# Kernel tuning notes

Measured on AMD Instinct MI355X. Metric: run time of the kernel, lower is better.

The kernel has to match this reference:

```python
import jax, jax.numpy as jnp
import numpy as np

B, N_SRC, N_NGH, D, H = 256, 32, 2048, 128, 2
DK = D // H  # 64
FEAT = 128
NEG_INF = -1e10
LN_EPS = 1e-5


def setup_inputs() -> dict:
    key = jax.random.key(0)
    ks = jax.random.split(key, 16)
    inp = {
        "src": jax.random.normal(ks[0], (B, N_SRC, D), jnp.float32),
        "ngh_feat": jax.random.normal(ks[1], (B * N_NGH, D), jnp.float32),
        "hidden": jnp.zeros((B * N_NGH, D), jnp.float32),
        "mask": jax.random.bernoulli(ks[2], 0.5, (B, N_NGH)),
        # GRUCell params (torch layout: [3H, in], gate order r,z,n)
        "gru_w_ih": jax.random.normal(ks[3], (3 * D, D), jnp.float32) * 0.05,
        "gru_w_hh": jax.random.normal(ks[4], (3 * D, D), jnp.float32) * 0.05,
        "gru_b_ih": jnp.zeros((3 * D,), jnp.float32),
        "gru_b_hh": jnp.zeros((3 * D,), jnp.float32),
        # multi-head attention projections (no bias in source)
        "w_qs": jax.random.normal(ks[5], (H * DK, D), jnp.float32) * np.sqrt(2.0 / (D + DK)).astype(np.float32),
        "w_ks": jax.random.normal(ks[6], (H * DK, D), jnp.float32) * np.sqrt(2.0 / (D + DK)).astype(np.float32),
        "w_vs": jax.random.normal(ks[7], (H * DK, D), jnp.float32) * np.sqrt(2.0 / (D + DK)).astype(np.float32),
        "fc_w": jax.random.normal(ks[8], (D, H * DK), jnp.float32) * 0.05,
        "fc_b": jnp.zeros((D,), jnp.float32),
        "ln_g": jnp.ones((D,), jnp.float32),
        "ln_b": jnp.zeros((D,), jnp.float32),
        # MergeLayer(model_dim, model_dim, feat_dim, feat_dim)
        "m_fc1_w": jax.random.normal(ks[9], (FEAT, 2 * D), jnp.float32) * 0.05,
        "m_fc1_b": jnp.zeros((FEAT,), jnp.float32),
        "m_fc2_w": jax.random.normal(ks[10], (FEAT, FEAT), jnp.float32) * 0.05,
        "m_fc2_b": jnp.zeros((FEAT,), jnp.float32),
    }
    return inp


def gru_cell(x, h, w_ih, w_hh, b_ih, b_hh):
    gi = x @ w_ih.T + b_ih
    gh = h @ w_hh.T + b_hh
    ir, iz, in_ = jnp.split(gi, 3, axis=-1)
    hr, hz, hn = jnp.split(gh, 3, axis=-1)
    r = jax.nn.sigmoid(ir + hr)
    z = jax.nn.sigmoid(iz + hz)
    n = jnp.tanh(in_ + r * hn)
    return (1.0 - z) * n + z * h


def reference(src, ngh_feat, hidden, mask,
              gru_w_ih, gru_w_hh, gru_b_ih, gru_b_hh,
              w_qs, w_ks, w_vs, fc_w, fc_b, ln_g, ln_b,
              m_fc1_w, m_fc1_b, m_fc2_w, m_fc2_b):
    b, n_src, d = src.shape
    n_ngh = mask.shape[1]
    nn = n_ngh // n_src  # neighbors per source
    temperature = jnp.sqrt(jnp.float32(DK))

    # GRU walk encoding of neighbor features -> seq [B, N_ngh, D]
    seq = gru_cell(ngh_feat, hidden, gru_w_ih, gru_w_hh, gru_b_ih, gru_b_hh)
    seq = seq.reshape(b, n_ngh, d)

    # grouped multi-head attention (q per source, k/v over its nn neighbors)
    q = (src @ w_qs.T).reshape(b, n_src, H, DK)            # bshd
    k = (seq @ w_ks.T).reshape(b, n_src, nn, H, DK)        # bsnhd
    v = (seq @ w_vs.T).reshape(b, n_src, nn, H, DK)
    scores = jnp.einsum('bshd,bsnhd->bshn', q, k) / temperature
    m = mask.reshape(b, n_src, 1, nn)                      # broadcast over heads
    scores = jnp.where(m, NEG_INF, scores)
    attn = jax.nn.softmax(scores, axis=-1)                 # dropout is eval no-op
    out = jnp.einsum('bshn,bsnhd->bshd', attn, v).reshape(b, n_src, H * DK)
    out = out @ fc_w.T + fc_b

    # residual + layernorm
    x = out + src
    mu = jnp.mean(x, axis=-1, keepdims=True)
    var = jnp.var(x, axis=-1, keepdims=True)
    x = (x - mu) * jax.lax.rsqrt(var + LN_EPS) * ln_g + ln_b

    # MergeLayer: cat + MLP
    cat = jnp.concatenate([x, src], axis=-1)
    h1 = jax.nn.relu(cat @ m_fc1_w.T + m_fc1_b)
    z = h1 @ m_fc2_w.T + m_fc2_b                            # [B, N_src, feat_dim]
    return z
```

## Files before the change

### kernel.cpp

```cpp
#include <hip/hip_runtime.h>

typedef float  f32x4  __attribute__((ext_vector_type(4)));
typedef short  bf16x8 __attribute__((ext_vector_type(8)));
typedef unsigned short u16x4 __attribute__((ext_vector_type(4)));

typedef const __attribute__((address_space(1))) unsigned int* gas_u32;
typedef __attribute__((address_space(3))) unsigned int* las_u32;

#define MFMA16(a,b,c) __builtin_amdgcn_mfma_f32_16x16x32_bf16((a),(b),(c),0,0,0)

__device__ __forceinline__ unsigned short f2bf(float f){
  unsigned u = __float_as_uint(f);
  u += 0x7fffu + ((u>>16)&1u);
  return (unsigned short)(u>>16);
}
__device__ __forceinline__ float bf2f(unsigned short u){
  return __uint_as_float(((unsigned)u)<<16);
}
__device__ __forceinline__ float sigm(float x){
  return __fdividef(1.f, 1.f + __expf(-x));
}
__device__ __forceinline__ float tanhfast(float x){
  return 1.f - __fdividef(2.f, __expf(2.f*x) + 1.f);
}
__device__ __forceinline__ float dot128(const float* __restrict__ w, const float* s){
  float a0=0.f,a1=0.f,a2=0.f,a3=0.f;
  #pragma unroll
  for (int e=0;e<32;++e){
    f32x4 w4 = *(const f32x4*)(w + (e<<2));
    f32x4 x4 = *(const f32x4*)(s + (e<<2));
    a0 = fmaf(w4[0],x4[0],a0); a1 = fmaf(w4[1],x4[1],a1);
    a2 = fmaf(w4[2],x4[2],a2); a3 = fmaf(w4[3],x4[3],a3);
  }
  return (a0+a1)+(a2+a3);
}
__device__ __forceinline__ bf16x8 cvt8(const f32x4 a, const f32x4 b){
  union { int i[4]; bf16x8 v; } u;
  asm("v_cvt_pk_bf16_f32 %0, %1, %2" : "=v"(u.i[0]) : "v"(a[0]), "v"(a[1]));
  asm("v_cvt_pk_bf16_f32 %0, %1, %2" : "=v"(u.i[1]) : "v"(a[2]), "v"(a[3]));
  asm("v_cvt_pk_bf16_f32 %0, %1, %2" : "=v"(u.i[2]) : "v"(b[0]), "v"(b[1]));
  asm("v_cvt_pk_bf16_f32 %0, %1, %2" : "=v"(u.i[3]) : "v"(b[2]), "v"(b[3]));
  return u.v;
}
__device__ __forceinline__ u16x4 pack4(float a, float b, float c, float d){
  union { int i[2]; u16x4 v; } u;
  asm("v_cvt_pk_bf16_f32 %0, %1, %2" : "=v"(u.i[0]) : "v"(a), "v"(b));
  asm("v_cvt_pk_bf16_f32 %0, %1, %2" : "=v"(u.i[1]) : "v"(c), "v"(d));
  return u.v;
}
__device__ __forceinline__ int swx(int m){ return (((m&7)<<1) | ((m>>3)&1)) << 2; }
__device__ __forceinline__ int sws(int m){ return ((m&7)<<3) | (((m>>3)&1)<<6); }

#define XB_OFF   0
#define SEQ_OFF  24576
#define QKB_OFF  40960
#define SC_OFF   43008
#define SH_OFF   43520
#define BIAS_OFF 47616
#define SMEM_SZ  49664

__global__ void prep_all(const float* __restrict__ wih, const float* __restrict__ whh,
                         const float* __restrict__ wqs, const float* __restrict__ wks,
                         const float* __restrict__ wvs, const float* __restrict__ fcw,
                         const float* __restrict__ src, const int* __restrict__ mask_i,
                         const float* __restrict__ hid,
                         unsigned short* __restrict__ wbf, float* __restrict__ M_ws,
                         unsigned short* __restrict__ qk_ws,
                         unsigned long long* __restrict__ mask_bits,
                         int* __restrict__ flags){
  __shared__ __align__(16) float sl_src[32*128];
  __shared__ __align__(16) float sl_q[32*128];
  const int b = blockIdx.x, t = threadIdx.x;
  if (b < 384){
    const int tid = b*256 + t;
    if (tid < 49152) wbf[tid] = f2bf(wih[tid]);
    else             wbf[tid] = f2bf(whh[tid-49152]);
  } else if (b < 512){
    const int tid = (b-384)*256 + t;
    const int h = tid>>14, d = (tid>>7)&127, e = tid&127;
    float a = 0.f;
    for (int j=0;j<64;++j)
      a = fmaf(fcw[d*128 + (h<<6) + j], wvs[((h<<6)+j)*128 + e], a);
    M_ws[tid] = a;
  } else if (b < 768){
    const int blk = b - 512;
    const size_t s0 = (size_t)blk * 32;
    for (int i=0;i<16;++i) sl_src[t + i*256] = src[s0*128 + t + i*256];
    __syncthreads();
    for (int k=0;k<16;++k){
      const int job = t + k*256, s = job>>7, c = job&127;
      sl_q[job] = dot128(wqs + c*128, sl_src + s*128);
    }
    __syncthreads();
    const int d = t&127, h = (t>>7)&1;
    float acc[32];
    #pragma unroll
    for (int s=0;s<32;++s) acc[s]=0.f;
    for (int j=0;j<64;++j){
      const float wk = wks[((h<<6)+j)*128 + d];
      #pragma unroll
      for (int s=0;s<32;++s) acc[s] = fmaf(wk, sl_q[s*128 + (h<<6) + j], acc[s]);
    }
    for (int s=0;s<32;++s) qk_ws[(s0+s)*256 + (h<<7) + d] = f2bf(acc[s]*0.125f);
  } else if (b < 2816){
    const int blk = b - 768;
    const int wv = t>>6, lane = t&63;
    const int gsrc = blk*4 + wv;
    const unsigned v = (unsigned)mask_i[(size_t)gsrc*64 + lane];
    const int bytemode = __any((int)(v > 1u));
    bool bit;
    if (bytemode) bit = (((const unsigned char*)mask_i)[(size_t)gsrc*64 + lane] != 0);
    else          bit = (v != 0u);
    const unsigned long long bits = __ballot((int)bit);
    if (lane == 0) mask_bits[gsrc] = bits;
  } else {
    const size_t blk = b - 2816;
    bool nz = false;
    #pragma unroll 4
    for (int it=0; it<32; ++it){
      const size_t idx = blk*8192 + (size_t)it*256 + t;
      const f32x4 v = *(const f32x4*)(hid + idx*4);
      nz = nz || (v[0]!=0.f)||(v[1]!=0.f)||(v[2]!=0.f)||(v[3]!=0.f);
    }
    if (__ballot((int)nz)){ if ((t&63)==0) atomicOr(flags+1, 1); }
  }
}

__device__ __forceinline__ void scores_pv(char* smem, int srcI, unsigned long long mb,
                                          int wv, int lane, int l15, int lgrp){
  unsigned short* seq = (unsigned short*)(smem + SEQ_OFF);
  const unsigned short* qkb = (const unsigned short*)(smem + QKB_OFF);
  float* sc = (float*)(smem + SC_OFF);
  float* sH = (float*)(smem + SH_OFF);
  const f32x4 z4 = {0.f,0.f,0.f,0.f};
  {
    const int srow = (wv<<4) + l15;
    f32x4 s4 = z4;
    #pragma unroll
    for (int kb=0;kb<4;++kb){
      const int ko = (kb<<5) + (lgrp<<3);
      bf16x8 qa = *(const bf16x8*)&qkb[(srcI<<8) + ((l15&1)<<7) + ko];
      bf16x8 sb = *(const bf16x8*)&seq[(srow<<7) + (ko ^ sws(srow))];
      s4 = MFMA16(qa, sb, s4);
    }
    if (lgrp == 0){
      sc[      (wv<<4) + l15] = s4[0];
      sc[64 +  (wv<<4) + l15] = s4[1];
    }
  }
  asm volatile("s_waitcnt lgkmcnt(0)" ::: "memory");
  __builtin_amdgcn_sched_barrier(0);
  __builtin_amdgcn_s_barrier();
  if (wv < 2){
    float s = ((mb>>lane)&1ull) ? -1e10f : sc[(wv<<6)+lane];
    float mx = s;
    #pragma unroll
    for (int o=32;o>=1;o>>=1) mx = fmaxf(mx, __shfl_xor(mx,o));
    const float e = __expf(s - mx);
    float sum = e;
    #pragma unroll
    for (int o=32;o>=1;o>>=1) sum += __shfl_xor(sum,o);
    sc[(wv<<6)+lane] = __fdividef(e, sum);
  }
  asm volatile("s_waitcnt lgkmcnt(0)" ::: "memory");
  __builtin_amdgcn_sched_barrier(0);
  __builtin_amdgcn_s_barrier();
  {
    const int tt = (wv<<6) + lane;
    const int jidx = tt>>2, sub = tt&3;
    const int hh2 = jidx>>5, quad = jidx&31;
    f32x4 a = z4;
    #pragma unroll
    for (int i=0;i<16;++i){
      const int rr = (sub<<4)+i;
      const u16x4 sv = *(const u16x4*)&seq[(rr<<7) + ((quad<<2) ^ sws(rr))];
      const float w = sc[(hh2<<6)+rr];
      #pragma unroll
      for (int k=0;k<4;++k) a[k] = fmaf(w, bf2f(sv[k]), a[k]);
    }
    #pragma unroll
    for (int k=0;k<4;++k){ a[k] += __shfl_xor(a[k],1); a[k] += __shfl_xor(a[k],2); }
    if (sub == 0)
      *(f32x4*)&sH[(((srcI<<1)+hh2)<<7) + (quad<<2)] = a;
  }
}

__global__ __attribute__((amdgpu_flat_work_group_size(256,256)))
           __attribute__((amdgpu_waves_per_eu(2)))
void cawn_main(
    const float* __restrict__ src, const float* __restrict__ ngh,
    const float* __restrict__ hid,
    const float* __restrict__ bih, const float* __restrict__ bhh,
    const float* __restrict__ fcb, const float* __restrict__ lng,
    const float* __restrict__ lnb, const float* __restrict__ m1w,
    const float* __restrict__ m1b, const float* __restrict__ m2w,
    const float* __restrict__ m2b,
    const unsigned short* __restrict__ wihb, const unsigned short* __restrict__ whhb,
    const float* __restrict__ M_ws, const unsigned short* __restrict__ qk_ws,
    const unsigned long long* __restrict__ mask_bits,
    const int* __restrict__ flags, float* __restrict__ out)
{
  __shared__ __align__(16) char smem[SMEM_SZ];
  float* brz0   = (float*)(smem + BIAS_OFF);
  float* brz1   = (float*)(smem + BIAS_OFF + 512);
  float* bin_l  = (float*)(smem + BIAS_OFF + 1024);
  float* bhn_l  = (float*)(smem + BIAS_OFF + 1536);
  unsigned short* seq = (unsigned short*)(smem + SEQ_OFF);
  unsigned short* qkb = (unsigned short*)(smem + QKB_OFF);

  const int t    = threadIdx.x;
  const int wv   = t >> 6;
  const int lane = t & 63;
  const int l15  = lane & 15;
  const int lgrp = lane >> 4;
  const int gsrc0 = blockIdx.x * 4;
  const f32x4 z4 = {0.f,0.f,0.f,0.f};
  const int hz = flags[1];

  if (t < 128){
    brz0[t]  = bih[t]     + bhh[t];
    brz1[t]  = bih[128+t] + bhh[128+t];
    bin_l[t] = bih[256+t];
    bhn_l[t] = bhh[256+t];
  }
  #pragma unroll
  for (int s=0;s<4;++s)
    qkb[(s<<8)+t] = qk_ws[(size_t)(gsrc0+s)*256 + t];
  const unsigned long long mb0 = mask_bits[gsrc0];
  const unsigned long long mb1 = mask_bits[gsrc0+1];
  const unsigned long long mb2 = mask_bits[gsrc0+2];
  const unsigned long long mb3 = mask_bits[gsrc0+3];

  if (!hz){
    bf16x8 Wf[3][2][4];
    #pragma unroll
    for (int g=0; g<3; ++g)
      #pragma unroll
      for (int j=0; j<2; ++j){
        const int nc = (wv<<5) + (j<<4) + l15;
        #pragma unroll
        for (int kb=0; kb<4; ++kb)
          Wf[g][j][kb] = *(const bf16x8*)(wihb + (((g<<7) + nc)<<7) + (kb<<5) + (lgrp<<3));
      }

    auto issue = [&](int kk, int rbuf){
      const int srcI = kk>>2, stg = kk&3;
      const size_t base = (size_t)(gsrc0+srcI)*8192 + (size_t)stg*2048;
      #pragma unroll
      for (int r=0;r<2;++r){
        const int rl = (wv<<2) + (r<<1) + (lane>>5);
        const int s16 = (lane&31) ^ (((rl&7)<<1) | ((rl>>3)&1));
        const float* g = ngh + base + (rl<<7) + (s16<<2);
        char* l = smem + XB_OFF + rbuf*8192 + (((wv<<2)+(r<<1))<<9);
        __builtin_amdgcn_global_load_lds((gas_u32)g, (las_u32)l, 16, 0, 0);
      }
    };
    issue(0,0); issue(1,1);

    int rb = 0;
    for (int k=0;k<16;++k){
      if (k < 15) asm volatile("s_waitcnt vmcnt(2) lgkmcnt(0)" ::: "memory");
      else        asm volatile("s_waitcnt vmcnt(0) lgkmcnt(0)" ::: "memory");
      __builtin_amdgcn_sched_barrier(0);
      __builtin_amdgcn_s_barrier();
      if (k+2 < 16){
        int ri = rb+2; if (ri>=3) ri-=3;
        issue(k+2, ri);
      }

      const int srcI = k>>2, stg = k&3;
      const float* xrow = (const float*)(smem + XB_OFF + rb*8192) + (l15<<7);
      const int sw = swx(l15);
      bf16x8 bx[4];
      #pragma unroll
      for (int kb=0;kb<4;++kb){
        const int c0 = (kb<<5) + (lgrp<<3);
        bx[kb] = cvt8(*(const f32x4*)&xrow[c0 ^ sw], *(const f32x4*)&xrow[(c0+4) ^ sw]);
      }
      f32x4 ar[2]={z4,z4}, az[2]={z4,z4}, an[2]={z4,z4};
      #pragma unroll
      for (int j=0;j<2;++j)
        #pragma unroll
        for (int kb=0;kb<4;++kb){
          ar[j] = MFMA16(Wf[0][j][kb], bx[kb], ar[j]);
          az[j] = MFMA16(Wf[1][j][kb], bx[kb], az[j]);
          an[j] = MFMA16(Wf[2][j][kb], bx[kb], an[j]);
        }
      const int mrow = (stg<<4) + l15;
      #pragma unroll
      for (int j=0;j<2;++j){
        const int colb = (wv<<5) + (j<<4) + (lgrp<<2);
        const f32x4 b0 = *(const f32x4*)&brz0[colb];
        const f32x4 b1 = *(const f32x4*)&brz1[colb];
        const f32x4 b2 = *(const f32x4*)&bin_l[colb];
        const f32x4 b3 = *(const f32x4*)&bhn_l[colb];
        float o[4];
        #pragma unroll
        for (int i=0;i<4;++i){
          const float rv = sigm(ar[j][i] + b0[i]);
          const float zv = sigm(az[j][i] + b1[i]);
          const float nv = tanhfast(an[j][i] + b2[i] + rv*b3[i]);
          o[i] = (1.f - zv)*nv;
        }
        *(u16x4*)&seq[(mrow<<7) + (colb ^ sws(mrow))] = pack4(o[0],o[1],o[2],o[3]);
      }

      if (stg == 3){
        asm volatile("s_waitcnt lgkmcnt(0)" ::: "memory");
        __builtin_amdgcn_sched_barrier(0);
        __builtin_amdgcn_s_barrier();
        const unsigned long long mb = (srcI==0)?mb0:(srcI==1)?mb1:(srcI==2)?mb2:mb3;
        scores_pv(smem, srcI, mb, wv, lane, l15, lgrp);
      }
      rb = (rb+1 == 3) ? 0 : rb+1;
    }
  } else {
    float* xb0 = (float*)(smem + XB_OFF);
    float* xb1 = (float*)(smem + XB_OFF + 8192);
    for (int srcI=0;srcI<4;++srcI){
      const int gsrc = gsrc0+srcI;
      for (int stg=0;stg<4;++stg){
        #pragma unroll
        for (int it=0; it<2; ++it){
          const int f = t + (it<<8);
          const int m = f>>5, c0 = (f&31)<<2;
          const int sw = swx(m);
          const size_t gb = (size_t)gsrc*8192 + stg*2048 + (m<<7) + c0;
          *(f32x4*)&xb0[(m<<7)+(c0^sw)] = *(const f32x4*)(ngh+gb);
          *(f32x4*)&xb1[(m<<7)+(c0^sw)] = *(const f32x4*)(hid+gb);
        }
        __syncthreads();
        const float* xrow = xb0 + (l15<<7);
        const float* hrow = xb1 + (l15<<7);
        const int sw = swx(l15);
        bf16x8 bx[4], bh[4];
        #pragma unroll
        for (int kb=0;kb<4;++kb){
          const int c0 = (kb<<5) + (lgrp<<3);
          bx[kb] = cvt8(*(const f32x4*)&xrow[c0 ^ sw], *(const f32x4*)&xrow[(c0+4) ^ sw]);
          bh[kb] = cvt8(*(const f32x4*)&hrow[c0 ^ sw], *(const f32x4*)&hrow[(c0+4) ^ sw]);
        }
        f32x4 ar[2]={z4,z4}, az[2]={z4,z4}, an[2]={z4,z4}, anh[2]={z4,z4};
        #pragma unroll
        for (int j=0;j<2;++j){
          const int nc = (wv<<5)+(j<<4)+l15;
          #pragma unroll
          for (int kb=0;kb<4;++kb){
            const int ko=(kb<<5)+(lgrp<<3);
            bf16x8 w0 = *(const bf16x8*)(wihb + ((      nc)<<7) + ko);
            bf16x8 w1 = *(const bf16x8*)(wihb + (((128)+nc)<<7) + ko);
            bf16x8 w2 = *(const bf16x8*)(wihb + (((256)+nc)<<7) + ko);
            ar[j] = MFMA16(w0, bx[kb], ar[j]);
            az[j] = MFMA16(w1, bx[kb], az[j]);
            an[j] = MFMA16(w2, bx[kb], an[j]);
            bf16x8 u0 = *(const bf16x8*)(whhb + ((      nc)<<7) + ko);
            bf16x8 u1 = *(const bf16x8*)(whhb + (((128)+nc)<<7) + ko);
            bf16x8 u2 = *(const bf16x8*)(whhb + (((256)+nc)<<7) + ko);
            ar[j]  = MFMA16(u0, bh[kb], ar[j]);
            az[j]  = MFMA16(u1, bh[kb], az[j]);
            anh[j] = MFMA16(u2, bh[kb], anh[j]);
          }
        }
        const int mrow = (stg<<4) + l15;
        #pragma unroll
        for (int j=0;j<2;++j){
          const int colb = (wv<<5) + (j<<4) + (lgrp<<2);
          const f32x4 b0 = *(const f32x4*)&brz0[colb];
          const f32x4 b1 = *(const f32x4*)&brz1[colb];
          const f32x4 b2 = *(const f32x4*)&bin_l[colb];
          const f32x4 b3 = *(const f32x4*)&bhn_l[colb];
          const f32x4 hv = *(const f32x4*)&hrow[colb ^ sw];
          float o[4];
          #pragma unroll
          for (int i=0;i<4;++i){
            const float rv = sigm(ar[j][i] + b0[i]);
            const float zv = sigm(az[j][i] + b1[i]);
            const float nv = tanhfast(an[j][i] + b2[i] + rv*(anh[j][i] + b3[i]));
            o[i] = (1.f - zv)*nv + zv*hv[i];
          }
          *(u16x4*)&seq[(mrow<<7) + (colb ^ sws(mrow))] = pack4(o[0],o[1],o[2],o[3]);
        }
        __syncthreads();
      }
      const unsigned long long mb = (srcI==0)?mb0:(srcI==1)?mb1:(srcI==2)?mb2:mb3;
      scores_pv(smem, srcI, mb, wv, lane, l15, lgrp);
      __syncthreads();
    }
  }

  __syncthreads();
  float* ep1  = (float*)smem;
  float* ep2  = (float*)(smem + 2048);
  float* srce = (float*)(smem + 4096);
  float* sH   = (float*)(smem + SH_OFF);
  srce[t]     = src[(size_t)gsrc0*128 + t];
  srce[t+256] = src[(size_t)gsrc0*128 + t + 256];
  __syncthreads();

  const int d  = t & 127;
  const int sh = (t >> 7) << 1;
  #pragma unroll
  for (int si=0; si<2; ++si){
    const int s = sh + si;
    float a = fcb[d];
    a += dot128(M_ws +         d*128, &sH[((s<<1)  )<<7]);
    a += dot128(M_ws + 16384 + d*128, &sH[((s<<1)+1)<<7]);
    ep1[s*128+d] = a + srce[s*128+d];
  }
  __syncthreads();
  {
    const int s = wv;
    const float v0 = ep1[s*128+lane], v1 = ep1[s*128+64+lane];
    float sum = v0+v1, sq_ = v0*v0 + v1*v1;
    #pragma unroll
    for (int o=32;o>=1;o>>=1){ sum += __shfl_xor(sum,o); sq_ += __shfl_xor(sq_,o); }
    const float mu  = sum * 0.0078125f;
    const float var = sq_ * 0.0078125f - mu*mu;
    const float rs  = rsqrtf(var + 1e-5f);
    ep1[s*128+lane]    = (v0-mu)*rs*lng[lane]    + lnb[lane];
    ep1[s*128+64+lane] = (v1-mu)*rs*lng[64+lane] + lnb[64+lane];
  }
  __syncthreads();
  #pragma unroll
  for (int si=0; si<2; ++si){
    const int s = sh + si;
    float a = m1b[d];
    a += dot128(m1w + d*256,       ep1  + s*128);
    a += dot128(m1w + d*256 + 128, srce + s*128);
    ep2[s*128+d] = fmaxf(a, 0.f);
  }
  __syncthreads();
  #pragma unroll
  for (int si=0; si<2; ++si){
    const int s = sh + si;
    out[(size_t)(gsrc0+s)*128 + d] = m2b[d] + dot128(m2w + d*128, ep2 + s*128);
  }
}

extern "C" void kernel_launch(void* const* d_in, const int* in_sizes, int n_in,
                              void* d_out, int out_size, void* d_ws, size_t ws_size,
                              hipStream_t stream){
  const float* src = (const float*)d_in[0];
  const float* ngh = (const float*)d_in[1];
  const float* hid = (const float*)d_in[2];
  const int*   msk = (const int*)  d_in[3];
  const float* wih = (const float*)d_in[4];
  const float* whh = (const float*)d_in[5];
  const float* bih = (const float*)d_in[6];
  const float* bhh = (const float*)d_in[7];
  const float* wqs = (const float*)d_in[8];
  const float* wks = (const float*)d_in[9];
  const float* wvs = (const float*)d_in[10];
  const float* fcw = (const float*)d_in[11];
  const float* fcb = (const float*)d_in[12];
  const float* lng = (const float*)d_in[13];
  const float* lnb = (const float*)d_in[14];
  const float* m1w = (const float*)d_in[15];
  const float* m1b = (const float*)d_in[16];
  const float* m2w = (const float*)d_in[17];
  const float* m2b = (const float*)d_in[18];
  float* out = (float*)d_out;

  unsigned short* wbf   = (unsigned short*)d_ws;
  int*            flags = (int*)((char*)d_ws + 196608);
  float*          M_ws  = (float*)((char*)d_ws + 196672);
  unsigned short* qk_ws = (unsigned short*)((char*)d_ws + 327744);
  unsigned long long* mask_bits = (unsigned long long*)((char*)d_ws + 4522048);

  hipMemsetAsync((char*)d_ws + 196608, 0, 64, stream);
  prep_all <<<4864, 256, 0, stream>>>(wih, whh, wqs, wks, wvs, fcw, src, msk, hid,
                                      wbf, M_ws, qk_ws, mask_bits, flags);
  cawn_main<<<2048, 256, 0, stream>>>(src, ngh, hid, bih, bhh,
                                      fcb, lng, lnb, m1w, m1b, m2w, m2b,
                                      wbf, wbf + 49152, M_ws, qk_ws,
                                      mask_bits, flags, out);
}
```

Baseline: 438.6 us.

## Split zero-hidden and general GRU paths into separate kernels, load inputs directly

Splits the main kernel into a fast kernel for the zero-hidden case and a slow kernel for the general case. Each kernel exits early based on a runtime flag. The fast kernel drops the triple-buffered global_load_lds staging of neighbor features and loads them straight from global memory into registers. This cuts shared memory per block from about 49 KB to about 25 KB to raise occupancy, at the cost of losing the async prefetch overlap and adding a second kernel launch that does no work.

Measured after the change: 545.9 us. 24.5% more time.

```diff
diff --git a/kernel.cpp b/kernel.cpp
--- a/kernel.cpp
+++ b/kernel.cpp
@@ -3,9 +3,6 @@
 typedef float  f32x4  __attribute__((ext_vector_type(4)));
 typedef short  bf16x8 __attribute__((ext_vector_type(8)));
 typedef unsigned short u16x4 __attribute__((ext_vector_type(4)));
-
-typedef const __attribute__((address_space(1))) unsigned int* gas_u32;
-typedef __attribute__((address_space(3))) unsigned int* las_u32;
 
 #define MFMA16(a,b,c) __builtin_amdgcn_mfma_f32_16x16x32_bf16((a),(b),(c),0,0,0)
 
@@ -48,16 +45,22 @@
   asm("v_cvt_pk_bf16_f32 %0, %1, %2" : "=v"(u.i[1]) : "v"(c), "v"(d));
   return u.v;
 }
+__device__ __forceinline__ int sws(int m){ return ((m&7)<<3) | (((m>>3)&1)<<6); }
 __device__ __forceinline__ int swx(int m){ return (((m&7)<<1) | ((m>>3)&1)) << 2; }
-__device__ __forceinline__ int sws(int m){ return ((m&7)<<3) | (((m>>3)&1)<<6); }
-
-#define XB_OFF   0
-#define SEQ_OFF  24576
-#define QKB_OFF  40960
-#define SC_OFF   43008
-#define SH_OFF   43520
-#define BIAS_OFF 47616
-#define SMEM_SZ  49664
+
+__device__ __forceinline__ void bar_lgkm(){
+  asm volatile("s_waitcnt lgkmcnt(0)" ::: "memory");
+  __builtin_amdgcn_sched_barrier(0);
+  __builtin_amdgcn_s_barrier();
+}
+
+#define SEQ_OFF  0
+#define QKB_OFF  16384
+#define SC_OFF   18432
+#define SH_OFF   18944
+#define BIAS_OFF 23040
+#define SMEM_FAST 25088
+#define SMEM_SLOW 41472
 
 __global__ void prep_all(const float* __restrict__ wih, const float* __restrict__ whh,
                          const float* __restrict__ wqs, const float* __restrict__ wks,
@@ -148,9 +151,7 @@
       sc[64 +  (wv<<4) + l15] = s4[1];
     }
   }
-  asm volatile("s_waitcnt lgkmcnt(0)" ::: "memory");
-  __builtin_amdgcn_sched_barrier(0);
-  __builtin_amdgcn_s_barrier();
+  bar_lgkm();
   if (wv < 2){
     float s = ((mb>>lane)&1ull) ? -1e10f : sc[(wv<<6)+lane];
     float mx = s;
@@ -162,9 +163,7 @@
     for (int o=32;o>=1;o>>=1) sum += __shfl_xor(sum,o);
     sc[(wv<<6)+lane] = __fdividef(e, sum);
   }
-  asm volatile("s_waitcnt lgkmcnt(0)" ::: "memory");
-  __builtin_amdgcn_sched_barrier(0);
-  __builtin_amdgcn_s_barrier();
+  bar_lgkm();
   {
     const int tt = (wv<<6) + lane;
     const int jidx = tt>>2, sub = tt&3;
@@ -185,22 +184,76 @@
   }
 }
 
+__device__ __forceinline__ void epilogue(char* smem, int t, int wv, int lane, int gsrc0,
+    const float* __restrict__ src, const float* __restrict__ fcb,
+    const float* __restrict__ lng, const float* __restrict__ lnb,
+    const float* __restrict__ m1w, const float* __restrict__ m1b,
+    const float* __restrict__ m2w, const float* __restrict__ m2b,
+    const float* __restrict__ M_ws, float* __restrict__ out){
+  float* ep1  = (float*)smem;
+  float* ep2  = (float*)(smem + 2048);
+  float* srce = (float*)(smem + 4096);
+  float* sH   = (float*)(smem + SH_OFF);
+  srce[t]     = src[(size_t)gsrc0*128 + t];
+  srce[t+256] = src[(size_t)gsrc0*128 + t + 256];
+  __syncthreads();
+
+  const int d  = t & 127;
+  const int sh = (t >> 7) << 1;
+  #pragma unroll
+  for (int si=0; si<2; ++si){
+    const int s = sh + si;
+    float a = fcb[d];
+    a += dot128(M_ws +         d*128, &sH[((s<<1)  )<<7]);
+    a += dot128(M_ws + 16384 + d*128, &sH[((s<<1)+1)<<7]);
+    ep1[s*128+d] = a + srce[s*128+d];
+  }
+  __syncthreads();
+  {
+    const int s = wv;
+    const float v0 = ep1[s*128+lane], v1 = ep1[s*128+64+lane];
+    float sum = v0+v1, sq_ = v0*v0 + v1*v1;
+    #pragma unroll
+    for (int o=32;o>=1;o>>=1){ sum += __shfl_xor(sum,o); sq_ += __shfl_xor(sq_,o); }
+    const float mu  = sum * 0.0078125f;
+    const float var = sq_ * 0.0078125f - mu*mu;
+    const float rs  = rsqrtf(var + 1e-5f);
+    ep1[s*128+lane]    = (v0-mu)*rs*lng[lane]    + lnb[lane];
+    ep1[s*128+64+lane] = (v1-mu)*rs*lng[64+lane] + lnb[64+lane];
+  }
+  __syncthreads();
+  #pragma unroll
+  for (int si=0; si<2; ++si){
+    const int s = sh + si;
+    float a = m1b[d];
+    a += dot128(m1w + d*256,       ep1  + s*128);
+    a += dot128(m1w + d*256 + 128, srce + s*128);
+    ep2[s*128+d] = fmaxf(a, 0.f);
+  }
+  __syncthreads();
+  #pragma unroll
+  for (int si=0; si<2; ++si){
+    const int s = sh + si;
+    out[(size_t)(gsrc0+s)*128 + d] = m2b[d] + dot128(m2w + d*128, ep2 + s*128);
+  }
+}
+
 __global__ __attribute__((amdgpu_flat_work_group_size(256,256)))
            __attribute__((amdgpu_waves_per_eu(2)))
-void cawn_main(
+void cawn_fast(
     const float* __restrict__ src, const float* __restrict__ ngh,
-    const float* __restrict__ hid,
     const float* __restrict__ bih, const float* __restrict__ bhh,
     const float* __restrict__ fcb, const float* __restrict__ lng,
     const float* __restrict__ lnb, const float* __restrict__ m1w,
     const float* __restrict__ m1b, const float* __restrict__ m2w,
     const float* __restrict__ m2b,
-    const unsigned short* __restrict__ wihb, const unsigned short* __restrict__ whhb,
+    const unsigned short* __restrict__ wihb,
     const float* __restrict__ M_ws, const unsigned short* __restrict__ qk_ws,
     const unsigned long long* __restrict__ mask_bits,
     const int* __restrict__ flags, float* __restrict__ out)
 {
-  __shared__ __align__(16) char smem[SMEM_SZ];
+  if (flags[1]) return;
+  __shared__ __align__(16) char smem[SMEM_FAST];
   float* brz0   = (float*)(smem + BIAS_OFF);
   float* brz1   = (float*)(smem + BIAS_OFF + 512);
   float* bin_l  = (float*)(smem + BIAS_OFF + 1024);
@@ -215,7 +268,6 @@
   const int lgrp = lane >> 4;
   const int gsrc0 = blockIdx.x * 4;
   const f32x4 z4 = {0.f,0.f,0.f,0.f};
-  const int hz = flags[1];
 
   if (t < 128){
     brz0[t]  = bih[t]     + bhh[t];
@@ -226,57 +278,29 @@
   #pragma unroll
   for (int s=0;s<4;++s)
     qkb[(s<<8)+t] = qk_ws[(size_t)(gsrc0+s)*256 + t];
-  const unsigned long long mb0 = mask_bits[gsrc0];
-  const unsigned long long mb1 = mask_bits[gsrc0+1];
-  const unsigned long long mb2 = mask_bits[gsrc0+2];
-  const unsigned long long mb3 = mask_bits[gsrc0+3];
-
-  if (!hz){
-    bf16x8 Wf[3][2][4];
-    #pragma unroll
-    for (int g=0; g<3; ++g)
-      #pragma unroll
-      for (int j=0; j<2; ++j){
-        const int nc = (wv<<5) + (j<<4) + l15;
-        #pragma unroll
-        for (int kb=0; kb<4; ++kb)
-          Wf[g][j][kb] = *(const bf16x8*)(wihb + (((g<<7) + nc)<<7) + (kb<<5) + (lgrp<<3));
-      }
-
-    auto issue = [&](int kk, int rbuf){
-      const int srcI = kk>>2, stg = kk&3;
-      const size_t base = (size_t)(gsrc0+srcI)*8192 + (size_t)stg*2048;
-      #pragma unroll
-      for (int r=0;r<2;++r){
-        const int rl = (wv<<2) + (r<<1) + (lane>>5);
-        const int s16 = (lane&31) ^ (((rl&7)<<1) | ((rl>>3)&1));
-        const float* g = ngh + base + (rl<<7) + (s16<<2);
-        char* l = smem + XB_OFF + rbuf*8192 + (((wv<<2)+(r<<1))<<9);
-        __builtin_amdgcn_global_load_lds((gas_u32)g, (las_u32)l, 16, 0, 0);
-      }
-    };
-    issue(0,0); issue(1,1);
-
-    int rb = 0;
-    for (int k=0;k<16;++k){
-      if (k < 15) asm volatile("s_waitcnt vmcnt(2) lgkmcnt(0)" ::: "memory");
-      else        asm volatile("s_waitcnt vmcnt(0) lgkmcnt(0)" ::: "memory");
-      __builtin_amdgcn_sched_barrier(0);
-      __builtin_amdgcn_s_barrier();
-      if (k+2 < 16){
-        int ri = rb+2; if (ri>=3) ri-=3;
-        issue(k+2, ri);
-      }
-
-      const int srcI = k>>2, stg = k&3;
-      const float* xrow = (const float*)(smem + XB_OFF + rb*8192) + (l15<<7);
-      const int sw = swx(l15);
+
+  bf16x8 Wf[3][2][4];
+  #pragma unroll
+  for (int g=0; g<3; ++g)
+    #pragma unroll
+    for (int j=0; j<2; ++j){
+      const int nc = (wv<<5) + (j<<4) + l15;
+      #pragma unroll
+      for (int kb=0; kb<4; ++kb)
+        Wf[g][j][kb] = *(const bf16x8*)(wihb + (((g<<7) + nc)<<7) + (kb<<5) + (lgrp<<3));
+    }
+  bar_lgkm();
+
+  for (int sI=0; sI<4; ++sI){
+    const float* xsrc = ngh + (size_t)(gsrc0+sI)*8192;
+    #pragma unroll 1
+    for (int rt=0; rt<4; ++rt){
+      const int row = (rt<<4) + l15;
+      const float* xg = xsrc + (row<<7) + (lgrp<<3);
       bf16x8 bx[4];
       #pragma unroll
-      for (int kb=0;kb<4;++kb){
-        const int c0 = (kb<<5) + (lgrp<<3);
-        bx[kb] = cvt8(*(const f32x4*)&xrow[c0 ^ sw], *(const f32x4*)&xrow[(c0+4) ^ sw]);
-      }
+      for (int kb=0;kb<4;++kb)
+        bx[kb] = cvt8(*(const f32x4*)(xg + (kb<<5)), *(const f32x4*)(xg + (kb<<5) + 4));
       f32x4 ar[2]={z4,z4}, az[2]={z4,z4}, an[2]={z4,z4};
       #pragma unroll
       for (int j=0;j<2;++j)
@@ -286,7 +310,6 @@
           az[j] = MFMA16(Wf[1][j][kb], bx[kb], az[j]);
           an[j] = MFMA16(Wf[2][j][kb], bx[kb], an[j]);
         }
-      const int mrow = (stg<<4) + l15;
       #pragma unroll
       for (int j=0;j<2;++j){
         const int colb = (wv<<5) + (j<<4) + (lgrp<<2);
@@ -302,139 +325,125 @@
           const float nv = tanhfast(an[j][i] + b2[i] + rv*b3[i]);
           o[i] = (1.f - zv)*nv;
         }
+        *(u16x4*)&seq[(row<<7) + (colb ^ sws(row))] = pack4(o[0],o[1],o[2],o[3]);
+      }
+    }
+    bar_lgkm();
+    scores_pv(smem, sI, mask_bits[gsrc0+sI], wv, lane, l15, lgrp);
+    bar_lgkm();
+  }
+
+  epilogue(smem, t, wv, lane, gsrc0, src, fcb, lng, lnb, m1w, m1b, m2w, m2b, M_ws, out);
+}
+
+__global__ __attribute__((amdgpu_flat_work_group_size(256,256)))
+           __attribute__((amdgpu_waves_per_eu(2)))
+void cawn_slow(
+    const float* __restrict__ src, const float* __restrict__ ngh,
+    const float* __restrict__ hid,
+    const float* __restrict__ bih, const float* __restrict__ bhh,
+    const float* __restrict__ fcb, const float* __restrict__ lng,
+    const float* __restrict__ lnb, const float* __restrict__ m1w,
+    const float* __restrict__ m1b, const float* __restrict__ m2w,
+    const float* __restrict__ m2b,
+    const unsigned short* __restrict__ wihb, const unsigned short* __restrict__ whhb,
+    const float* __restrict__ M_ws, const unsigned short* __restrict__ qk_ws,
+    const unsigned long long* __restrict__ mask_bits,
+    const int* __restrict__ flags, float* __restrict__ out)
+{
+  if (!flags[1]) return;
+  __shared__ __align__(16) char smem[SMEM_SLOW];
+  float* brz0   = (float*)(smem + BIAS_OFF);
+  float* brz1   = (float*)(smem + BIAS_OFF + 512);
+  float* bin_l  = (float*)(smem + BIAS_OFF + 1024);
+  float* bhn_l  = (float*)(smem + BIAS_OFF + 1536);
+  unsigned short* seq = (unsigned short*)(smem + SEQ_OFF);
+  unsigned short* qkb = (unsigned short*)(smem + QKB_OFF);
+  float* xb0 = (float*)(smem + 25088);
+  float* xb1 = (float*)(smem + 33280);
+
+  const int t    = threadIdx.x;
+  const int wv   = t >> 6;
+  const int lane = t & 63;
+  const int l15  = lane & 15;
+  const int lgrp = lane >> 4;
+  const int gsrc0 = blockIdx.x * 4;
+  const f32x4 z4 = {0.f,0.f,0.f,0.f};
+
+  if (t < 128){
+    brz0[t]  = bih[t]     + bhh[t];
+    brz1[t]  = bih[128+t] + bhh[128+t];
+    bin_l[t] = bih[256+t];
+    bhn_l[t] = bhh[256+t];
+  }
+  #pragma unroll
+  for (int sI=0;sI<4;++sI)
+    qkb[(sI<<8)+t] = qk_ws[(size_t)(gsrc0+sI)*256 + t];
+
+  for (int srcI=0;srcI<4;++srcI){
+    const int gsrc = gsrc0+srcI;
+    for (int stg=0;stg<4;++stg){
+      #pragma unroll
+      for (int it=0; it<2; ++it){
+        const int f = t + (it<<8);
+        const int m = f>>5, c0 = (f&31)<<2;
+        const int sw = swx(m);
+        const size_t gb = (size_t)gsrc*8192 + stg*2048 + (m<<7) + c0;
+        *(f32x4*)&xb0[(m<<7)+(c0^sw)] = *(const f32x4*)(ngh+gb);
+        *(f32x4*)&xb1[(m<<7)+(c0^sw)] = *(const f32x4*)(hid+gb);
+      }
+      __syncthreads();
+      const float* xrow = xb0 + (l15<<7);
+      const float* hrow = xb1 + (l15<<7);
+      const int sw = swx(l15);
+      bf16x8 bx[4], bh[4];
+      #pragma unroll
+      for (int kb=0;kb<4;++kb){
+        const int c0 = (kb<<5) + (lgrp<<3);
+        bx[kb] = cvt8(*(const f32x4*)&xrow[c0 ^ sw], *(const f32x4*)&xrow[(c0+4) ^ sw]);
+        bh[kb] = cvt8(*(const f32x4*)&hrow[c0 ^ sw], *(const f32x4*)&hrow[(c0+4) ^ sw]);
+      }
+      f32x4 ar[2]={z4,z4}, az[2]={z4,z4}, an[2]={z4,z4}, anh[2]={z4,z4};
+      #pragma unroll
+      for (int j=0;j<2;++j){
+        const int nc = (wv<<5)+(j<<4)+l15;
+        #pragma unroll
+        for (int kb=0;kb<4;++kb){
+          const int ko=(kb<<5)+(lgrp<<3);
+          ar[j] = MFMA16(*(const bf16x8*)(wihb + ((      nc)<<7) + ko), bx[kb], ar[j]);
+          az[j] = MFMA16(*(const bf16x8*)(wihb + (((128)+nc)<<7) + ko), bx[kb], az[j]);
+          an[j] = MFMA16(*(const bf16x8*)(wihb + (((256)+nc)<<7) + ko), bx[kb], an[j]);
+          ar[j]  = MFMA16(*(const bf16x8*)(whhb + ((      nc)<<7) + ko), bh[kb], ar[j]);
+          az[j]  = MFMA16(*(const bf16x8*)(whhb + (((128)+nc)<<7) + ko), bh[kb], az[j]);
+          anh[j] = MFMA16(*(const bf16x8*)(whhb + (((256)+nc)<<7) + ko), bh[kb], anh[j]);
+        }
+      }
+      const int mrow = (stg<<4) + l15;
+      #pragma unroll
+      for (int j=0;j<2;++j){
+        const int colb = (wv<<5) + (j<<4) + (lgrp<<2);
+        const f32x4 b0 = *(const f32x4*)&brz0[colb];
+        const f32x4 b1 = *(const f32x4*)&brz1[colb];
+        const f32x4 b2 = *(const f32x4*)&bin_l[colb];
+        const f32x4 b3 = *(const f32x4*)&bhn_l[colb];
+        const f32x4 hv = *(const f32x4*)&hrow[colb ^ sw];
+        float o[4];
+        #pragma unroll
+        for (int i=0;i<4;++i){
+          const float rv = sigm(ar[j][i] + b0[i]);
+          const float zv = sigm(az[j][i] + b1[i]);
+          const float nv = tanhfast(an[j][i] + b2[i] + rv*(anh[j][i] + b3[i]));
+          o[i] = (1.f - zv)*nv + zv*hv[i];
+        }
         *(u16x4*)&seq[(mrow<<7) + (colb ^ sws(mrow))] = pack4(o[0],o[1],o[2],o[3]);
       }
-
-      if (stg == 3){
-        asm volatile("s_waitcnt lgkmcnt(0)" ::: "memory");
-        __builtin_amdgcn_sched_barrier(0);
-        __builtin_amdgcn_s_barrier();
-        const unsigned long long mb = (srcI==0)?mb0:(srcI==1)?mb1:(srcI==2)?mb2:mb3;
-        scores_pv(smem, srcI, mb, wv, lane, l15, lgrp);
-      }
-      rb = (rb+1 == 3) ? 0 : rb+1;
-    }
-  } else {
-    float* xb0 = (float*)(smem + XB_OFF);
-    float* xb1 = (float*)(smem + XB_OFF + 8192);
-    for (int srcI=0;srcI<4;++srcI){
-      const int gsrc = gsrc0+srcI;
-      for (int stg=0;stg<4;++stg){
-        #pragma unroll
-        for (int it=0; it<2; ++it){
-          const int f = t + (it<<8);
-          const int m = f>>5, c0 = (f&31)<<2;
-          const int sw = swx(m);
-          const size_t gb = (size_t)gsrc*8192 + stg*2048 + (m<<7) + c0;
-          *(f32x4*)&xb0[(m<<7)+(c0^sw)] = *(const f32x4*)(ngh+gb);
-          *(f32x4*)&xb1[(m<<7)+(c0^sw)] = *(const f32x4*)(hid+gb);
-        }
-        __syncthreads();
-        const float* xrow = xb0 + (l15<<7);
-        const float* hrow = xb1 + (l15<<7);
-        const int sw = swx(l15);
-        bf16x8 bx[4], bh[4];
-        #pragma unroll
-        for (int kb=0;kb<4;++kb){
-          const int c0 = (kb<<5) + (lgrp<<3);
-          bx[kb] = cvt8(*(const f32x4*)&xrow[c0 ^ sw], *(const f32x4*)&xrow[(c0+4) ^ sw]);
-          bh[kb] = cvt8(*(const f32x4*)&hrow[c0 ^ sw], *(const f32x4*)&hrow[(c0+4) ^ sw]);
-        }
-        f32x4 ar[2]={z4,z4}, az[2]={z4,z4}, an[2]={z4,z4}, anh[2]={z4,z4};
-        #pragma unroll
-        for (int j=0;j<2;++j){
-          const int nc = (wv<<5)+(j<<4)+l15;
-          #pragma unroll
-          for (int kb=0;kb<4;++kb){
-            const int ko=(kb<<5)+(lgrp<<3);
-            bf16x8 w0 = *(const bf16x8*)(wihb + ((      nc)<<7) + ko);
-            bf16x8 w1 = *(const bf16x8*)(wihb + (((128)+nc)<<7) + ko);
-            bf16x8 w2 = *(const bf16x8*)(wihb + (((256)+nc)<<7) + ko);
-            ar[j] = MFMA16(w0, bx[kb], ar[j]);
-            az[j] = MFMA16(w1, bx[kb], az[j]);
-            an[j] = MFMA16(w2, bx[kb], an[j]);
-            bf16x8 u0 = *(const bf16x8*)(whhb + ((      nc)<<7) + ko);
-            bf16x8 u1 = *(const bf16x8*)(whhb + (((128)+nc)<<7) + ko);
-            bf16x8 u2 = *(const bf16x8*)(whhb + (((256)+nc)<<7) + ko);
-            ar[j]  = MFMA16(u0, bh[kb], ar[j]);
-            az[j]  = MFMA16(u1, bh[kb], az[j]);
-            anh[j] = MFMA16(u2, bh[kb], anh[j]);
-          }
-        }
-        const int mrow = (stg<<4) + l15;
-        #pragma unroll
-        for (int j=0;j<2;++j){
-          const int colb = (wv<<5) + (j<<4) + (lgrp<<2);
-          const f32x4 b0 = *(const f32x4*)&brz0[colb];
-          const f32x4 b1 = *(const f32x4*)&brz1[colb];
-          const f32x4 b2 = *(const f32x4*)&bin_l[colb];
-          const f32x4 b3 = *(const f32x4*)&bhn_l[colb];
-          const f32x4 hv = *(const f32x4*)&hrow[colb ^ sw];
-          float o[4];
-          #pragma unroll
-          for (int i=0;i<4;++i){
-            const float rv = sigm(ar[j][i] + b0[i]);
-            const float zv = sigm(az[j][i] + b1[i]);
-            const float nv = tanhfast(an[j][i] + b2[i] + rv*(anh[j][i] + b3[i]));
-            o[i] = (1.f - zv)*nv + zv*hv[i];
-          }
-          *(u16x4*)&seq[(mrow<<7) + (colb ^ sws(mrow))] = pack4(o[0],o[1],o[2],o[3]);
-        }
-        __syncthreads();
-      }
-      const unsigned long long mb = (srcI==0)?mb0:(srcI==1)?mb1:(srcI==2)?mb2:mb3;
-      scores_pv(smem, srcI, mb, wv, lane, l15, lgrp);
       __syncthreads();
     }
-  }
-
-  __syncthreads();
-  float* ep1  = (float*)smem;
-  float* ep2  = (float*)(smem + 2048);
-  float* srce = (float*)(smem + 4096);
-  float* sH   = (float*)(smem + SH_OFF);
-  srce[t]     = src[(size_t)gsrc0*128 + t];
-  srce[t+256] = src[(size_t)gsrc0*128 + t + 256];
-  __syncthreads();
-
-  const int d  = t & 127;
-  const int sh = (t >> 7) << 1;
-  #pragma unroll
-  for (int si=0; si<2; ++si){
-    const int s = sh + si;
-    float a = fcb[d];
-    a += dot128(M_ws +         d*128, &sH[((s<<1)  )<<7]);
-    a += dot128(M_ws + 16384 + d*128, &sH[((s<<1)+1)<<7]);
-    ep1[s*128+d] = a + srce[s*128+d];
-  }
-  __syncthreads();
-  {
-    const int s = wv;
-    const float v0 = ep1[s*128+lane], v1 = ep1[s*128+64+lane];
-    float sum = v0+v1, sq_ = v0*v0 + v1*v1;
-    #pragma unroll
-    for (int o=32;o>=1;o>>=1){ sum += __shfl_xor(sum,o); sq_ += __shfl_xor(sq_,o); }
-    const float mu  = sum * 0.0078125f;
-    const float var = sq_ * 0.0078125f - mu*mu;
-    const float rs  = rsqrtf(var + 1e-5f);
-    ep1[s*128+lane]    = (v0-mu)*rs*lng[lane]    + lnb[lane];
-    ep1[s*128+64+lane] = (v1-mu)*rs*lng[64+lane] + lnb[64+lane];
-  }
-  __syncthreads();
-  #pragma unroll
-  for (int si=0; si<2; ++si){
-    const int s = sh + si;
-    float a = m1b[d];
-    a += dot128(m1w + d*256,       ep1  + s*128);
-    a += dot128(m1w + d*256 + 128, srce + s*128);
-    ep2[s*128+d] = fmaxf(a, 0.f);
-  }
-  __syncthreads();
-  #pragma unroll
-  for (int si=0; si<2; ++si){
-    const int s = sh + si;
-    out[(size_t)(gsrc0+s)*128 + d] = m2b[d] + dot128(m2w + d*128, ep2 + s*128);
-  }
+    scores_pv(smem, srcI, mask_bits[gsrc], wv, lane, l15, lgrp);
+    __syncthreads();
+  }
+
+  epilogue(smem, t, wv, lane, gsrc0, src, fcb, lng, lnb, m1w, m1b, m2w, m2b, M_ws, out);
 }
 
 extern "C" void kernel_launch(void* const* d_in, const int* in_sizes, int n_in,
@@ -470,7 +479,10 @@
   hipMemsetAsync((char*)d_ws + 196608, 0, 64, stream);
   prep_all <<<4864, 256, 0, stream>>>(wih, whh, wqs, wks, wvs, fcw, src, msk, hid,
                                       wbf, M_ws, qk_ws, mask_bits, flags);
-  cawn_main<<<2048, 256, 0, stream>>>(src, ngh, hid, bih, bhh,
+  cawn_fast<<<2048, 256, 0, stream>>>(src, ngh, bih, bhh,
+                                      fcb, lng, lnb, m1w, m1b, m2w, m2b,
+                                      wbf, M_ws, qk_ws, mask_bits, flags, out);
+  cawn_slow<<<2048, 256, 0, stream>>>(src, ngh, hid, bih, bhh,
                                       fcb, lng, lnb, m1w, m1b, m2w, m2b,
                                       wbf, wbf + 49152, M_ws, qk_ws,
                                       mask_bits, flags, out);
```
